# Optimization experiments

Measured on AMD Instinct MI355X. Metric: run time of the kernel, lower is better.

Reference implementation:

```python
import jax, jax.numpy as jnp
import numpy as np

EPS = 1e-20


def _conv(x, w, pad):
    # NCHW / OIHW conv, stride 1, symmetric padding
    return jax.lax.conv_general_dilated(
        x, w, window_strides=(1, 1),
        padding=((pad, pad), (pad, pad)),
        dimension_numbers=("NCHW", "OIHW", "NCHW"))


def _nconv(data, conf, w, b, pad):
    # normalized convolution: conv(d*c)/conv(c) + bias ; cout = conv(c)/sum(w)
    denom = _conv(conf, w, pad)
    nomin = _conv(data * conf, w, pad)
    out = nomin / (denom + EPS) + b[None, :, None, None]
    s = jnp.sum(w, axis=(1, 2, 3))  # per-out-channel kernel sum
    cout = denom / s[None, :, None, None]
    return out, cout


def _maxpool_ds(x, c):
    # 2x2/stride-2 max pool on c, gathering x at argmax positions (torch return_indices semantics)
    B, C, H, W = c.shape
    cw = c.reshape(B, C, H // 2, 2, W // 2, 2).transpose(0, 1, 2, 4, 3, 5).reshape(B, C, H // 2, W // 2, 4)
    xw = x.reshape(B, C, H // 2, 2, W // 2, 2).transpose(0, 1, 2, 4, 3, 5).reshape(B, C, H // 2, W // 2, 4)
    idx = jnp.argmax(cw, axis=-1)  # first-max tie-break, same as torch
    c_ds = jnp.take_along_axis(cw, idx[..., None], axis=-1)[..., 0] / 4.0
    x_ds = jnp.take_along_axis(xw, idx[..., None], axis=-1)[..., 0]
    return x_ds, c_ds


def _up2(x):
    return jnp.repeat(jnp.repeat(x, 2, axis=2), 2, axis=3)


def setup_inputs() -> dict:
    key = jax.random.key(0)
    ks = jax.random.split(key, 18)
    B, H, W = 8, 512, 512
    x0 = jax.random.normal(ks[0], (B, 1, H, W), dtype=jnp.float32)
    c0 = jax.random.uniform(ks[1], (B, 1, H, W), dtype=jnp.float32)

    def posw(k, shape):
        # positive kernel (the module enforces positivity via softplus hook)
        return jax.nn.softplus(jax.random.normal(k, shape, dtype=jnp.float32))

    inp = {"x0": x0, "c0": c0}
    shapes = {
        "w1": (2, 1, 5, 5), "w2": (2, 2, 5, 5), "w3": (2, 2, 5, 5),
        "w4": (2, 4, 3, 3), "w5": (2, 4, 3, 3), "w6": (2, 4, 3, 3),
        "w7": (1, 2, 1, 1),
    }
    for i, (name, shp) in enumerate(shapes.items()):
        inp[name] = posw(ks[2 + i], shp)
        inp["b" + name[1:]] = jnp.full((shp[0],), 0.01, dtype=jnp.float32)
    return inp


def reference(x0, c0, w1, b1, w2, b2, w3, b3, w4, b4, w5, b5, w6, b6, w7, b7):
    x1, c1 = _nconv(x0, c0, w1, b1, 2)
    x1, c1 = _nconv(x1, c1, w2, b2, 2)
    x1, c1 = _nconv(x1, c1, w3, b3, 2)

    x1_ds, c1_ds = _maxpool_ds(x1, c1)
    x2_ds, c2_ds = _nconv(x1_ds, c1_ds, w2, b2, 2)
    x2_ds, c2_ds = _nconv(x2_ds, c2_ds, w3, b3, 2)

    x2_dss, c2_dss = _maxpool_ds(x2_ds, c2_ds)
    x3_ds, c3_ds = _nconv(x2_dss, c2_dss, w2, b2, 2)

    x3_dss, c3_dss = _maxpool_ds(x3_ds, c3_ds)
    x4_ds, c4_ds = _nconv(x3_dss, c3_dss, w2, b2, 2)

    x4, c4 = _up2(x4_ds), _up2(c4_ds)
    x34_ds, c34_ds = _nconv(jnp.concatenate((x3_ds, x4), 1), jnp.concatenate((c3_ds, c4), 1), w4, b4, 1)

    x34, c34 = _up2(x34_ds), _up2(c34_ds)
    x23_ds, c23_ds = _nconv(jnp.concatenate((x2_ds, x34), 1), jnp.concatenate((c2_ds, c34), 1), w5, b5, 1)

    x23, c23 = _up2(x23_ds), _up2(c23_ds)
    xout, cout = _nconv(jnp.concatenate((x23, x1), 1), jnp.concatenate((c23, c1), 1), w6, b6, 1)
    xout, cout = _nconv(xout, cout, w7, b7, 0)
    return xout, cout
```

## Files before the change

kernel.cpp:

```cpp
#include <hip/hip_runtime.h>

#define EPSF 1e-20f

typedef float v2f __attribute__((ext_vector_type(2)));

__device__ __forceinline__ float frcp(float x) { return __builtin_amdgcn_rcpf(x); }


struct CD8 { v2f v[8]; };
__device__ __forceinline__ CD8 load_cd8(const float2* p) {
    const float4* q = (const float4*)p;
    const float4 t0 = q[0], t1 = q[1], t2 = q[2], t3 = q[3];
    CD8 r;
    r.v[0] = (v2f){t0.x, t0.y}; r.v[1] = (v2f){t0.z, t0.w};
    r.v[2] = (v2f){t1.x, t1.y}; r.v[3] = (v2f){t1.z, t1.w};
    r.v[4] = (v2f){t2.x, t2.y}; r.v[5] = (v2f){t2.z, t2.w};
    r.v[6] = (v2f){t3.x, t3.y}; r.v[7] = (v2f){t3.z, t3.w};
    return r;
}
struct CD6 { v2f v[6]; };
__device__ __forceinline__ CD6 load_cd6(const float2* p) {
    const float4* q = (const float4*)p;
    const float4 t0 = q[0], t1 = q[1], t2 = q[2];
    CD6 r;
    r.v[0] = (v2f){t0.x, t0.y}; r.v[1] = (v2f){t0.z, t0.w};
    r.v[2] = (v2f){t1.x, t1.y}; r.v[3] = (v2f){t1.z, t1.w};
    r.v[4] = (v2f){t2.x, t2.y}; r.v[5] = (v2f){t2.z, t2.w};
    return r;
}
__device__ __forceinline__ void fma2(v2f& a, float w, v2f cd) {
    a = __builtin_elementwise_fma((v2f){w, w}, cd, a);
}

template<int NCI, int CI0, int CINT, int K, int ROWS>
__device__ __forceinline__ void conv_core_i(const float2* __restrict__ s,
                                            const float* __restrict__ wgt,
                                            int lh, int lw,
                                            v2f acc[2][4])
{
    constexpr int JB = 2 - (K / 2);
    #pragma unroll
    for (int kh = 0; kh < K; ++kh) {
        #pragma unroll
        for (int ci = 0; ci < NCI; ++ci) {
            const CD8 cd = load_cd8(s + (ci * ROWS + lh + kh) * 72 + lw + 2);
            #pragma unroll
            for (int kw = 0; kw < K; ++kw) {
                const float w0 = wgt[((0 * CINT + CI0 + ci) * K + kh) * K + kw];
                const float w1 = wgt[((1 * CINT + CI0 + ci) * K + kh) * K + kw];
                #pragma unroll
                for (int p = 0; p < 4; ++p) {
                    const int j = p + kw + JB;
                    fma2(acc[0][p], w0, cd.v[j]);
                    fma2(acc[1][p], w1, cd.v[j]);
                }
            }
        }
    }
}

template<int LO0>
__device__ __forceinline__ void conv_low_i(const float2* __restrict__ s_lo,
                                           const float* __restrict__ wgt,
                                           int lh, int lw,
                                           v2f acc[2][4])
{
    #pragma unroll
    for (int kh = 0; kh < 3; ++kh) {
        const int rel_r = ((lh + kh - 1) >> 1) + 1;
        #pragma unroll
        for (int lci = 0; lci < 2; ++lci) {
            const CD6 cd = load_cd6(s_lo + (lci * 10 + rel_r) * 40 + (lw >> 1) + 2);
            #pragma unroll
            for (int kw = 0; kw < 3; ++kw) {
                const float w0 = wgt[((0 * 4 + LO0 + lci) * 3 + kh) * 3 + kw];
                const float w1 = wgt[((1 * 4 + LO0 + lci) * 3 + kh) * 3 + kw];
                #pragma unroll
                for (int p = 0; p < 4; ++p) {
                    const int t = p + kw - 1;
                    const int jl = ((t < 0) ? -1 : (t >> 1)) + 2;
                    fma2(acc[0][p], w0, cd.v[jl]);
                    fma2(acc[1][p], w1, cd.v[jl]);
                }
            }
        }
    }
}

template<int CINT, int K>
__device__ __forceinline__ void nconv_epilogue_i(const float* __restrict__ wgt,
                                                 const float* __restrict__ bias,
                                                 v2f acc[2][4],
                                                 float4 uo[2], float4 co4[2])
{
    #pragma unroll
    for (int c = 0; c < 2; ++c) {
        float s = 0.f;
        for (int i = 0; i < CINT * K * K; ++i) s += wgt[c * CINT * K * K + i];
        const float is = 1.0f / s;
        const float bb = bias[c];
        #pragma unroll
        for (int p = 0; p < 4; ++p) {
            const float xo = acc[c][p].y * frcp(acc[c][p].x + EPSF) + bb;
            const float cv = acc[c][p].x * is;
            (&co4[c].x)[p] = cv;
            (&uo[c].x)[p]  = xo * cv;
        }
    }
}

__global__ __launch_bounds__(256)
void enc12_fused(const float* __restrict__ x0, const float* __restrict__ c0,
                 const float* __restrict__ wA, const float* __restrict__ bA,
                 const float* __restrict__ wB, const float* __restrict__ bB,
                 float* __restrict__ uout, float* __restrict__ cout)
{
    __shared__ __align__(16) float2 in_cd[24][84];
    __shared__ __align__(16) float2 mid_cd[2][20][72];

    const int tid = threadIdx.x;
    const int bw = blockIdx.x * 64;
    const int bh = blockIdx.y * 16;
    const int b  = blockIdx.z;

    const float4* x4 = (const float4*)x0;
    const float4* c4 = (const float4*)c0;
    for (int i = tid; i < 480; i += 256) {
        const int r = i / 20, k = i % 20;
        const int gh = bh - 4 + r;
        const int gw4 = (bw >> 2) - 2 + k;
        float4 xx = make_float4(0.f, 0.f, 0.f, 0.f);
        float4 cc = make_float4(0.f, 0.f, 0.f, 0.f);
        if ((unsigned)gh < 512u && (unsigned)gw4 < 128u) {
            const int a = (b << 16) + (gh << 7) + gw4;
            xx = x4[a];
            cc = c4[a];
        }
        float4* dst = (float4*)&in_cd[r][4 * k];
        dst[0] = make_float4(cc.x, xx.x * cc.x, cc.y, xx.y * cc.y);
        dst[1] = make_float4(cc.z, xx.z * cc.z, cc.w, xx.w * cc.w);
    }

    float isA0, isA1;
    {
        float s0 = 0.f, s1 = 0.f;
        for (int i = 0; i < 25; ++i) { s0 += wA[i]; s1 += wA[25 + i]; }
        isA0 = 1.0f / s0;
        isA1 = 1.0f / s1;
    }
    __syncthreads();

    #pragma unroll
    for (int pass = 0; pass < 2; ++pass) {
        int r, g;
        bool active = true;
        if (pass == 0) { r = tid >> 4; g = tid & 15; }
        else {
            if (tid < 64) { r = 16 + (tid >> 4); g = tid & 15; }
            else if (tid < 104) { const int t = tid - 64; r = t >> 1; g = 16 + (t & 1); }
            else { active = false; r = 0; g = 0; }
        }
        if (active) {
            v2f acc[2][4];
            #pragma unroll
            for (int c = 0; c < 2; ++c)
                #pragma unroll
                for (int p = 0; p < 4; ++p) acc[c][p] = (v2f){0.f, 0.f};
            #pragma unroll
            for (int kh = 0; kh < 5; ++kh) {
                const CD8 cd = load_cd8(&in_cd[r + kh][4 * g + 2]);
                #pragma unroll
                for (int kw = 0; kw < 5; ++kw) {
                    const float w0 = wA[kh * 5 + kw];
                    const float w1 = wA[25 + kh * 5 + kw];
                    #pragma unroll
                    for (int p = 0; p < 4; ++p) {
                        fma2(acc[0][p], w0, cd.v[p + kw]);
                        fma2(acc[1][p], w1, cd.v[p + kw]);
                    }
                }
            }
            const int orow = bh + r - 2;
            const bool rok = (unsigned)orow < 512u;
            #pragma unroll
            for (int c = 0; c < 2; ++c) {
                const float is = (c == 0) ? isA0 : isA1;
                float cv[4], du[4];
                #pragma unroll
                for (int p = 0; p < 4; ++p) {
                    const int ocol = bw + 4 * g - 4 + p;
                    const bool ok = rok && (unsigned)ocol < 512u;
                    const float xo = acc[c][p].y * frcp(acc[c][p].x + EPSF) + bA[c];
                    const float v = acc[c][p].x * is;
                    cv[p] = ok ? v : 0.f;
                    du[p] = ok ? xo * v : 0.f;
                }
                float4* dst = (float4*)&mid_cd[c][r][4 * g];
                dst[0] = make_float4(cv[0], du[0], cv[1], du[1]);
                dst[1] = make_float4(cv[2], du[2], cv[3], du[3]);
            }
        }
    }
    __syncthreads();

    const int lh = tid >> 4;
    const int lw = (tid & 15) << 2;
    v2f acc[2][4];
    #pragma unroll
    for (int c = 0; c < 2; ++c)
        #pragma unroll
        for (int p = 0; p < 4; ++p) acc[c][p] = (v2f){0.f, 0.f};

    conv_core_i<2, 0, 2, 5, 20>(&mid_cd[0][0][0], wB, lh, lw, acc);

    float4 uo[2], co4[2];
    nconv_epilogue_i<2, 5>(wB, bB, acc, uo, co4);

    const int oh = bh + lh;
    #pragma unroll
    for (int c = 0; c < 2; ++c) {
        const int a = ((b * 2 + c) << 16) + (oh << 7) + ((bw + lw) >> 2);
        ((float4*)uout)[a] = uo[c];
        ((float4*)cout)[a] = co4[c];
    }
}

__global__ __launch_bounds__(256)
void enc45_fused(const float* __restrict__ inU, const float* __restrict__ inC,
                 const float* __restrict__ wA, const float* __restrict__ bA,
                 const float* __restrict__ wB, const float* __restrict__ bB,
                 float* __restrict__ uout, float* __restrict__ cout,
                 float* __restrict__ poolU, float* __restrict__ poolC)
{
    __shared__ __align__(16) float2 in_cd[2][24][84];
    __shared__ __align__(16) float2 mid_cd[2][20][72];

    const int tid = threadIdx.x;
    const int bw = blockIdx.x * 64;
    const int bh = blockIdx.y * 16;
    const int b  = blockIdx.z;

    const float4* U4 = (const float4*)inU;
    const float4* C4 = (const float4*)inC;
    for (int i = tid; i < 960; i += 256) {
        const int ci = i / 480;
        const int r = (i / 20) % 24, k = i % 20;
        const int gh = bh - 4 + r;
        const int gw4 = (bw >> 2) - 2 + k;
        float4 dd = make_float4(0.f, 0.f, 0.f, 0.f);
        float4 cc = make_float4(0.f, 0.f, 0.f, 0.f);
        if ((unsigned)gh < 256u && (unsigned)gw4 < 64u) {
            const int a = ((b * 2 + ci) << 14) + (gh << 6) + gw4;
            dd = U4[a];
            cc = C4[a];
        }
        float4* dst = (float4*)&in_cd[ci][r][4 * k];
        dst[0] = make_float4(cc.x, dd.x, cc.y, dd.y);
        dst[1] = make_float4(cc.z, dd.z, cc.w, dd.w);
    }

    float isA0, isA1;
    {
        float s0 = 0.f, s1 = 0.f;
        for (int i = 0; i < 50; ++i) { s0 += wA[i]; s1 += wA[50 + i]; }
        isA0 = 1.0f / s0;
        isA1 = 1.0f / s1;
    }
    __syncthreads();

    #pragma unroll
    for (int pass = 0; pass < 2; ++pass) {
        int r, g;
        bool active = true;
        if (pass == 0) { r = tid >> 4; g = tid & 15; }
        else {
            if (tid < 64) { r = 16 + (tid >> 4); g = tid & 15; }
            else if (tid < 104) { const int t = tid - 64; r = t >> 1; g = 16 + (t & 1); }
            else { active = false; r = 0; g = 0; }
        }
        if (active) {
            v2f acc[2][4];
            #pragma unroll
            for (int c = 0; c < 2; ++c)
                #pragma unroll
                for (int p = 0; p < 4; ++p) acc[c][p] = (v2f){0.f, 0.f};
            #pragma unroll
            for (int kh = 0; kh < 5; ++kh) {
                #pragma unroll
                for (int ci = 0; ci < 2; ++ci) {
                    const CD8 cd = load_cd8(&in_cd[ci][r + kh][4 * g + 2]);
                    #pragma unroll
                    for (int kw = 0; kw < 5; ++kw) {
                        const float w0 = wA[((0 * 2 + ci) * 5 + kh) * 5 + kw];
                        const float w1 = wA[((1 * 2 + ci) * 5 + kh) * 5 + kw];
                        #pragma unroll
                        for (int p = 0; p < 4; ++p) {
                            fma2(acc[0][p], w0, cd.v[p + kw]);
                            fma2(acc[1][p], w1, cd.v[p + kw]);
                        }
                    }
                }
            }
            const int orow = bh + r - 2;
            const bool rok = (unsigned)orow < 256u;
            #pragma unroll
            for (int c = 0; c < 2; ++c) {
                const float is = (c == 0) ? isA0 : isA1;
                float cv[4], du[4];
                #pragma unroll
                for (int p = 0; p < 4; ++p) {
                    const int ocol = bw + 4 * g - 4 + p;
                    const bool ok = rok && (unsigned)ocol < 256u;
                    const float xo = acc[c][p].y * frcp(acc[c][p].x + EPSF) + bA[c];
                    const float v = acc[c][p].x * is;
                    cv[p] = ok ? v : 0.f;
                    du[p] = ok ? xo * v : 0.f;
                }
                float4* dst = (float4*)&mid_cd[c][r][4 * g];
                dst[0] = make_float4(cv[0], du[0], cv[1], du[1]);
                dst[1] = make_float4(cv[2], du[2], cv[3], du[3]);
            }
        }
    }
    __syncthreads();

    const int lh = tid >> 4;
    const int lw = (tid & 15) << 2;
    v2f acc[2][4];
    #pragma unroll
    for (int c = 0; c < 2; ++c)
        #pragma unroll
        for (int p = 0; p < 4; ++p) acc[c][p] = (v2f){0.f, 0.f};

    conv_core_i<2, 0, 2, 5, 20>(&mid_cd[0][0][0], wB, lh, lw, acc);

    float4 uo[2], co4[2];
    nconv_epilogue_i<2, 5>(wB, bB, acc, uo, co4);

    const int oh = bh + lh;
    #pragma unroll
    for (int c = 0; c < 2; ++c) {
        const int a = ((b * 2 + c) << 14) + (oh << 6) + ((bw + lw) >> 2);
        ((float4*)uout)[a] = uo[c];
        ((float4*)cout)[a] = co4[c];
    }

    __syncthreads();
    float2* pb = &mid_cd[0][0][0];
    #pragma unroll
    for (int c = 0; c < 2; ++c) {
        float2* row = pb + (c * 16 + lh) * 64 + lw;
        #pragma unroll
        for (int p = 0; p < 4; ++p)
            row[p] = make_float2((&co4[c].x)[p], (&uo[c].x)[p]);
    }
    __syncthreads();
    #pragma unroll
    for (int rep = 0; rep < 2; ++rep) {
        const int o = tid + rep * 256;
        const int ch = o >> 8;
        const int idx = o & 255;
        const int pr = idx >> 5;
        const int pcc = idx & 31;
        const float2* base = pb + (ch * 16 + 2 * pr) * 64 + 2 * pcc;
        const float2 a0 = base[0], a1 = base[1], a2 = base[64], a3 = base[65];
        float m = a0.x, g = a0.y;
        if (a1.x > m) { m = a1.x; g = a1.y; }
        if (a2.x > m) { m = a2.x; g = a2.y; }
        if (a3.x > m) { m = a3.x; g = a3.y; }
        const int pa = ((b * 2 + ch) << 14) + (((bh >> 1) + pr) << 7) + (bw >> 1) + pcc;
        poolU[pa] = g * 0.25f;
        poolC[pa] = m * 0.25f;
    }
}

__global__ __launch_bounds__(256)
void mid_kern(const float* __restrict__ p2U, const float* __restrict__ p2C,
              const float* __restrict__ w2, const float* __restrict__ b2,
              const float* __restrict__ w4, const float* __restrict__ b4,
              float* __restrict__ x34U, float* __restrict__ x34C)
{
    __shared__ __align__(16) float2 sp_cd[2][32][88];
    __shared__ __align__(16) float2 sx3_cd[2][28][80];
    __shared__ __align__(16) float2 sp3_cd[2][14][48];
    __shared__ __align__(16) float2 sx4_cd[2][10][40];

    const int tid = threadIdx.x;
    const int bw = blockIdx.x * 64;
    const int bh = blockIdx.y * 16;
    const int b = blockIdx.z;

    const float4* U4 = (const float4*)p2U;
    const float4* C4 = (const float4*)p2C;
    for (int i = tid; i < 2 * 32 * 22; i += 256) {
        const int ci = i / 704;
        const int r  = (i / 22) % 32;
        const int cf = i % 22;
        const int gh = bh - 8 + r;
        const int gw4 = (bw >> 2) - 3 + cf;
        float4 dd = make_float4(0.f, 0.f, 0.f, 0.f);
        float4 cc = make_float4(0.f, 0.f, 0.f, 0.f);
        if ((unsigned)gh < 128u && (unsigned)gw4 < 32u) {
            const int a = ((b * 2 + ci) << 12) + (gh << 5) + gw4;
            dd = U4[a];
            cc = C4[a];
        }
        float4* dst = (float4*)&sp_cd[ci][r][cf * 4];
        dst[0] = make_float4(cc.x, dd.x, cc.y, dd.y);
        dst[1] = make_float4(cc.z, dd.z, cc.w, dd.w);
    }
    __syncthreads();

    {
        float s2[2];
        #pragma unroll
        for (int c = 0; c < 2; ++c) {
            float s = 0.f;
            for (int i = 0; i < 50; ++i) s += w2[c * 50 + i];
            s2[c] = 1.0f / s;
        }
        for (int s = tid; s < 560; s += 256) {
            const int r = s / 20;
            const int g = s % 20;
            v2f acc[2][4];
            #pragma unroll
            for (int c = 0; c < 2; ++c)
                #pragma unroll
                for (int p = 0; p < 4; ++p) acc[c][p] = (v2f){0.f, 0.f};
            #pragma unroll
            for (int kh = 0; kh < 5; ++kh) {
                #pragma unroll
                for (int ci = 0; ci < 2; ++ci) {
                    const CD8 cd = load_cd8(&sp_cd[ci][r + kh][4 * g + 2]);
                    #pragma unroll
                    for (int kw = 0; kw < 5; ++kw) {
                        const float w0 = w2[((0 * 2 + ci) * 5 + kh) * 5 + kw];
                        const float w1 = w2[((1 * 2 + ci) * 5 + kh) * 5 + kw];
                        #pragma unroll
                        for (int p = 0; p < 4; ++p) {
                            fma2(acc[0][p], w0, cd.v[p + kw]);
                            fma2(acc[1][p], w1, cd.v[p + kw]);
                        }
                    }
                }
            }
            const int orow = bh - 6 + r;
            const bool rok = (unsigned)orow < 128u;
            #pragma unroll
            for (int c = 0; c < 2; ++c) {
                float cv[4], du[4];
                #pragma unroll
                for (int p = 0; p < 4; ++p) {
                    const int ocol = bw - 8 + 4 * g + p;
                    const bool ok = rok && (unsigned)ocol < 128u;
                    const float xo = acc[c][p].y * frcp(acc[c][p].x + EPSF) + b2[c];
                    const float v = acc[c][p].x * s2[c];
                    cv[p] = ok ? v : 0.f;
                    du[p] = ok ? xo * v : 0.f;
                }
                float4* dst = (float4*)&sx3_cd[c][r][4 * g];
                dst[0] = make_float4(cv[0], du[0], cv[1], du[1]);
                dst[1] = make_float4(cv[2], du[2], cv[3], du[3]);
            }
        }
    }
    __syncthreads();

    for (int i = tid; i < 2 * 14 * 48; i += 256) {
        const int ch = i / 672;
        const int r  = (i / 48) % 14;
        const int c  = i % 48;
        const int R = (bh >> 1) - 3 + r;
        const int C = (bw >> 1) - 8 + c;
        float g = 0.f, m = 0.f;
        if (c >= 4 && c < 44 && (unsigned)R < 64u && (unsigned)C < 64u) {
            const int xr = 2 * r, xc = 2 * c - 8;
            const float2 a0 = sx3_cd[ch][xr][xc],     a1 = sx3_cd[ch][xr][xc + 1];
            const float2 a2 = sx3_cd[ch][xr + 1][xc], a3 = sx3_cd[ch][xr + 1][xc + 1];
            m = a0.x; g = a0.y;
            if (a1.x > m) { m = a1.x; g = a1.y; }
            if (a2.x > m) { m = a2.x; g = a2.y; }
            if (a3.x > m) { m = a3.x; g = a3.y; }
            g *= 0.25f; m *= 0.25f;
        }
        sp3_cd[ch][r][c] = make_float2(m, g);
    }
    __syncthreads();

    {
        float s2[2];
        #pragma unroll
        for (int c = 0; c < 2; ++c) {
            float s = 0.f;
            for (int i = 0; i < 50; ++i) s += w2[c * 50 + i];
            s2[c] = 1.0f / s;
        }
        for (int s = tid; s < 100; s += 256) {
            const int r = s / 10;
            const int g = s % 10;
            v2f acc[2][4];
            #pragma unroll
            for (int c = 0; c < 2; ++c)
                #pragma unroll
                for (int p = 0; p < 4; ++p) acc[c][p] = (v2f){0.f, 0.f};
            #pragma unroll
            for (int kh = 0; kh < 5; ++kh) {
                #pragma unroll
                for (int ci = 0; ci < 2; ++ci) {
                    const CD8 cd = load_cd8(&sp3_cd[ci][r + kh][4 * g + 2]);
                    #pragma unroll
                    for (int kw = 0; kw < 5; ++kw) {
                        const float w0 = w2[((0 * 2 + ci) * 5 + kh) * 5 + kw];
                        const float w1 = w2[((1 * 2 + ci) * 5 + kh) * 5 + kw];
                        #pragma unroll
                        for (int p = 0; p < 4; ++p) {
                            fma2(acc[0][p], w0, cd.v[p + kw]);
                            fma2(acc[1][p], w1, cd.v[p + kw]);
                        }
                    }
                }
            }
            const int orow = (bh >> 1) - 1 + r;
            const bool rok = (unsigned)orow < 64u;
            #pragma unroll
            for (int c = 0; c < 2; ++c) {
                float cv[4], du[4];
                #pragma unroll
                for (int p = 0; p < 4; ++p) {
                    const int ocol = (bw >> 1) - 4 + 4 * g + p;
                    const bool ok = rok && (unsigned)ocol < 64u;
                    const float xo = acc[c][p].y * frcp(acc[c][p].x + EPSF) + b2[c];
                    const float v = acc[c][p].x * s2[c];
                    cv[p] = ok ? v : 0.f;
                    du[p] = ok ? xo * v : 0.f;
                }
                float4* dst = (float4*)&sx4_cd[c][r][4 * g];
                dst[0] = make_float4(cv[0], du[0], cv[1], du[1]);
                dst[1] = make_float4(cv[2], du[2], cv[3], du[3]);
            }
        }
    }
    __syncthreads();

    {
        const int lh = tid >> 4;
        const int lw = (tid & 15) << 2;
        v2f acc[2][4];
        #pragma unroll
        for (int c = 0; c < 2; ++c)
            #pragma unroll
            for (int p = 0; p < 4; ++p) acc[c][p] = (v2f){0.f, 0.f};

        #pragma unroll
        for (int kh = 0; kh < 3; ++kh) {
            #pragma unroll
            for (int ci = 0; ci < 2; ++ci) {
                const CD8 cd = load_cd8(&sx3_cd[ci][lh + kh + 5][lw + 6]);
                #pragma unroll
                for (int kw = 0; kw < 3; ++kw) {
                    const float w0 = w4[((0 * 4 + ci) * 3 + kh) * 3 + kw];
                    const float w1 = w4[((1 * 4 + ci) * 3 + kh) * 3 + kw];
                    #pragma unroll
                    for (int p = 0; p < 4; ++p) {
                        const int j = p + kw + 1;
                        fma2(acc[0][p], w0, cd.v[j]);
                        fma2(acc[1][p], w1, cd.v[j]);
                    }
                }
            }
        }
        conv_low_i<2>(&sx4_cd[0][0][0], w4, lh, lw, acc);

        float4 uo[2], co4[2];
        nconv_epilogue_i<4, 3>(w4, b4, acc, uo, co4);
        #pragma unroll
        for (int c = 0; c < 2; ++c) {
            const int a = ((b * 2 + c) << 12) + ((bh + lh) << 5) + ((bw + lw) >> 2);
            ((float4*)x34U)[a] = uo[c];
            ((float4*)x34C)[a] = co4[c];
        }
    }
}

template<int CIN, int K, int LOGHW, bool IN_IS_U, bool POOL>
__global__ __launch_bounds__(256)
void nconv_tiled(const float* __restrict__ xin, const float* __restrict__ cin_,
                 const float* __restrict__ wgt, const float* __restrict__ bias,
                 float* __restrict__ uout, float* __restrict__ cout,
                 float* __restrict__ poolU, float* __restrict__ poolC)
{
    constexpr int HW = 1 << LOGHW;
    constexpr int PAD = K / 2;
    constexpr int TH = 16;
    constexpr int ROWS = TH + 2 * PAD;
    constexpr int NC4 = 18;
    __shared__ __align__(16) float2 s_cd[CIN][ROWS][72];

    const int tid = threadIdx.x;
    const int base_w = blockIdx.x * 64;
    const int base_h = blockIdx.y * TH;
    const int b = blockIdx.z;

    constexpr int SLOTS = CIN * ROWS * NC4;
    const float4* x4 = (const float4*)xin;
    const float4* c4p = (const float4*)cin_;
    for (int i = tid; i < SLOTS; i += 256) {
        const int ci = i / (ROWS * NC4);
        const int r  = (i / NC4) % ROWS;
        const int cf = i % NC4;
        const int gh = base_h - PAD + r;
        const int gw4 = (base_w >> 2) + cf - 1;
        float4 dd = make_float4(0.f, 0.f, 0.f, 0.f);
        float4 cc = make_float4(0.f, 0.f, 0.f, 0.f);
        if ((unsigned)gh < (unsigned)HW && (unsigned)gw4 < (unsigned)(HW >> 2)) {
            const int a = ((b * CIN + ci) << (2 * LOGHW - 2)) + (gh << (LOGHW - 2)) + gw4;
            const float4 xx = x4[a];
            cc = c4p[a];
            if (IN_IS_U) dd = xx;
            else dd = make_float4(xx.x * cc.x, xx.y * cc.y, xx.z * cc.z, xx.w * cc.w);
        }
        float4* dst = (float4*)&s_cd[ci][r][cf * 4];
        dst[0] = make_float4(cc.x, dd.x, cc.y, dd.y);
        dst[1] = make_float4(cc.z, dd.z, cc.w, dd.w);
    }
    __syncthreads();

    const int lh = tid >> 4;
    const int lw = (tid & 15) << 2;
    v2f acc[2][4];
    #pragma unroll
    for (int c = 0; c < 2; ++c)
        #pragma unroll
        for (int p = 0; p < 4; ++p) acc[c][p] = (v2f){0.f, 0.f};

    conv_core_i<CIN, 0, CIN, K, ROWS>(&s_cd[0][0][0], wgt, lh, lw, acc);

    float4 uo[2], co4[2];
    nconv_epilogue_i<CIN, K>(wgt, bias, acc, uo, co4);

    const int oh = base_h + lh;
    #pragma unroll
    for (int c = 0; c < 2; ++c) {
        const int a = ((b * 2 + c) << (2 * LOGHW - 2)) + (oh << (LOGHW - 2)) + ((base_w + lw) >> 2);
        ((float4*)uout)[a] = uo[c];
        ((float4*)cout)[a] = co4[c];
    }

    if (POOL) {
        __syncthreads();
        float2* pb = &s_cd[0][0][0];
        #pragma unroll
        for (int c = 0; c < 2; ++c) {
            float2* row = pb + (c * 16 + lh) * 64 + lw;
            #pragma unroll
            for (int p = 0; p < 4; ++p)
                row[p] = make_float2((&co4[c].x)[p], (&uo[c].x)[p]);
        }
        __syncthreads();
        #pragma unroll
        for (int rep = 0; rep < 2; ++rep) {
            const int o = tid + rep * 256;
            const int ch = o >> 8;
            const int idx = o & 255;
            const int pr = idx >> 5;
            const int pcc = idx & 31;
            const float2* base = pb + (ch * 16 + 2 * pr) * 64 + 2 * pcc;
            const float2 a0 = base[0], a1 = base[1], a2 = base[64], a3 = base[65];
            float m = a0.x, g = a0.y;
            if (a1.x > m) { m = a1.x; g = a1.y; }
            if (a2.x > m) { m = a2.x; g = a2.y; }
            if (a3.x > m) { m = a3.x; g = a3.y; }
            const int pa = ((b * 2 + ch) << (2 * (LOGHW - 1)))
                         + (((base_h >> 1) + pr) << (LOGHW - 1)) + (base_w >> 1) + pcc;
            poolU[pa] = g * 0.25f;
            poolC[pa] = m * 0.25f;
        }
    }
}

template<bool UP_FIRST, int LOGHW, bool FINAL>
__global__ __launch_bounds__(256)
void nconv_cat_tiled(const float* __restrict__ skU, const float* __restrict__ skC,
                     const float* __restrict__ loU, const float* __restrict__ loC,
                     const float* __restrict__ wgt, const float* __restrict__ bias,
                     float* __restrict__ uout, float* __restrict__ cout,
                     const float* __restrict__ w7, const float* __restrict__ b7)
{
    constexpr int HW = 1 << LOGHW;
    constexpr int HWL = HW >> 1;
    constexpr int TH = 16;
    constexpr int ROWS = TH + 2;
    constexpr int NC4 = 18;
    constexpr int SK0 = UP_FIRST ? 2 : 0;
    constexpr int LO0 = UP_FIRST ? 0 : 2;
    __shared__ __align__(16) float2 s_cd[2][ROWS][72];
    __shared__ __align__(16) float2 lo_cd[2][10][40];

    const int tid = threadIdx.x;
    const int base_w = blockIdx.x * 64;
    const int base_h = blockIdx.y * TH;
    const int b = blockIdx.z;

    constexpr int SLOTS = 2 * ROWS * NC4;
    const float4* sU4 = (const float4*)skU;
    const float4* sC4 = (const float4*)skC;
    for (int i = tid; i < SLOTS; i += 256) {
        const int ci = i / (ROWS * NC4);
        const int r  = (i / NC4) % ROWS;
        const int cf = i % NC4;
        const int gh = base_h - 1 + r;
        const int gw4 = (base_w >> 2) + cf - 1;
        float4 dd = make_float4(0.f, 0.f, 0.f, 0.f);
        float4 cc = make_float4(0.f, 0.f, 0.f, 0.f);
        if ((unsigned)gh < (unsigned)HW && (unsigned)gw4 < (unsigned)(HW >> 2)) {
            const int a = ((b * 2 + ci) << (2 * LOGHW - 2)) + (gh << (LOGHW - 2)) + gw4;
            dd = sU4[a];
            cc = sC4[a];
        }
        float4* dst = (float4*)&s_cd[ci][r][cf * 4];
        dst[0] = make_float4(cc.x, dd.x, cc.y, dd.y);
        dst[1] = make_float4(cc.z, dd.z, cc.w, dd.w);
    }
    constexpr int LO_SLOTS = 2 * 10 * 10;
    const int lo_r0 = (base_h >> 1) - 1;
    const int lo_c4_0 = (base_w >> 3) - 1;
    const float4* lU4 = (const float4*)loU;
    const float4* lC4 = (const float4*)loC;
    for (int i = tid; i < LO_SLOTS; i += 256) {
        const int ci = i / 100;
        const int r  = (i / 10) % 10;
        const int cf = i % 10;
        const int gr = lo_r0 + r;
        const int gc4 = lo_c4_0 + cf;
        float4 dd = make_float4(0.f, 0.f, 0.f, 0.f);
        float4 cc = make_float4(0.f, 0.f, 0.f, 0.f);
        if ((unsigned)gr < (unsigned)HWL && (unsigned)gc4 < (unsigned)(HWL >> 2)) {
            const int a = ((b * 2 + ci) << (2 * (LOGHW - 1) - 2)) + (gr << (LOGHW - 3)) + gc4;
            dd = lU4[a];
            cc = lC4[a];
        }
        float4* dst = (float4*)&lo_cd[ci][r][cf * 4];
        dst[0] = make_float4(cc.x, dd.x, cc.y, dd.y);
        dst[1] = make_float4(cc.z, dd.z, cc.w, dd.w);
    }
    __syncthreads();

    const int lh = tid >> 4;
    const int lw = (tid & 15) << 2;
    v2f acc[2][4];
    #pragma unroll
    for (int c = 0; c < 2; ++c)
        #pragma unroll
        for (int p = 0; p < 4; ++p) acc[c][p] = (v2f){0.f, 0.f};

    conv_core_i<2, SK0, 4, 3, ROWS>(&s_cd[0][0][0], wgt, lh, lw, acc);
    conv_low_i<LO0>(&lo_cd[0][0][0], wgt, lh, lw, acc);

    float4 uo[2], co4[2];
    nconv_epilogue_i<4, 3>(wgt, bias, acc, uo, co4);

    const int oh = base_h + lh;
    if (FINAL) {
        const float w70 = w7[0], w71 = w7[1], bb7 = b7[0];
        const float inv = frcp(w70 + w71);
        float4 xo4, cc4;
        #pragma unroll
        for (int p = 0; p < 4; ++p) {
            const float d1 = w70 * (&co4[0].x)[p] + w71 * (&co4[1].x)[p];
            (&xo4.x)[p] = (w70 * (&uo[0].x)[p] + w71 * (&uo[1].x)[p]) * frcp(d1 + EPSF) + bb7;
            (&cc4.x)[p] = d1 * inv;
        }
        const int a = (b << (2 * LOGHW - 2)) + (oh << (LOGHW - 2)) + ((base_w + lw) >> 2);
        ((float4*)uout)[a] = xo4;
        ((float4*)uout)[(1 << 19) + a] = cc4;
    } else {
        #pragma unroll
        for (int c = 0; c < 2; ++c) {
            const int a = ((b * 2 + c) << (2 * LOGHW - 2)) + (oh << (LOGHW - 2)) + ((base_w + lw) >> 2);
            ((float4*)uout)[a] = uo[c];
            ((float4*)cout)[a] = co4[c];
        }
    }
}

extern "C" void kernel_launch(void* const* d_in, const int* in_sizes, int n_in,
                              void* d_out, int out_size, void* d_ws, size_t ws_size,
                              hipStream_t stream) {
    (void)in_sizes; (void)n_in; (void)out_size; (void)ws_size;
    const float* x0 = (const float*)d_in[0];
    const float* c0 = (const float*)d_in[1];
    const float* w1 = (const float*)d_in[2];  const float* b1 = (const float*)d_in[3];
    const float* w2 = (const float*)d_in[4];  const float* b2 = (const float*)d_in[5];
    const float* w3 = (const float*)d_in[6];  const float* b3 = (const float*)d_in[7];
    const float* w4 = (const float*)d_in[8];  const float* b4 = (const float*)d_in[9];
    const float* w5 = (const float*)d_in[10]; const float* b5 = (const float*)d_in[11];
    const float* w6 = (const float*)d_in[12]; const float* b6 = (const float*)d_in[13];
    const float* w7 = (const float*)d_in[14]; const float* b7 = (const float*)d_in[15];

    float* ws = (float*)d_ws;
    const size_t S512 = 8ull * 2 * 512 * 512;
    const size_t S256 = 8ull * 2 * 256 * 256;
    const size_t S128 = 8ull * 2 * 128 * 128;

    float* X1x = ws;            float* X1c = ws + S512;
    float* Ax  = ws + 2 * S512;
    float* Bx  = ws + 4 * S512; float* Bc  = ws + 5 * S512;
    float* x23x = Ax;               float* x23c = Ax + S256;
    float* x2x  = Ax + 2 * S256;    float* x2c  = Ax + 3 * S256;
    float* p1x  = Ax + 4 * S256;    float* p1c  = Ax + 5 * S256;
    float* p2x  = Bx + 2 * S128;    float* p2c  = Bx + 3 * S128;
    float* x34x = Bx + 4 * S128;    float* x34c = Bx + 5 * S128;

    enc12_fused<<<dim3(8, 32, 8), 256, 0, stream>>>(
        x0, c0, w1, b1, w2, b2, Bx, Bc);
    nconv_tiled<2, 5, 9, true, true><<<dim3(8, 32, 8), 256, 0, stream>>>(
        Bx, Bc, w3, b3, X1x, X1c, p1x, p1c);
    enc45_fused<<<dim3(4, 16, 8), 256, 0, stream>>>(
        p1x, p1c, w2, b2, w3, b3, x2x, x2c, p2x, p2c);
    mid_kern<<<dim3(2, 8, 8), 256, 0, stream>>>(
        p2x, p2c, w2, b2, w4, b4, x34x, x34c);
    nconv_cat_tiled<false, 8, false><<<dim3(4, 16, 8), 256, 0, stream>>>(
        x2x, x2c, x34x, x34c, w5, b5, x23x, x23c, nullptr, nullptr);
    nconv_cat_tiled<true, 9, true><<<dim3(8, 32, 8), 256, 0, stream>>>(
        X1x, X1c, x23x, x23c, w6, b6, (float*)d_out, nullptr, w7, b7);
}
```

Baseline: 114.0 us.

## Register-block two output rows per thread and pool from registers in the first encoder stages

The first two full-resolution kernels now use 32-row tiles. Each thread computes two adjacent output rows, so every input row loaded from shared memory feeds both row accumulators, and the 5x5 halo is amortised over a taller tile. The third-conv kernel replaces the generic templated kernel and does the 2x2 max-pool directly from the thread's own register results. This removes the shared-memory staging pass and its two extra barriers. In exchange, accumulator registers double and enc12 needs about 67KB of shared memory, which may lower occupancy.

```diff
diff --git a/kernel.cpp b/kernel.cpp
--- a/kernel.cpp
+++ b/kernel.cpp
@@ -110,22 +110,23 @@
 }
 
 __global__ __launch_bounds__(256)
-void enc12_fused(const float* __restrict__ x0, const float* __restrict__ c0,
-                 const float* __restrict__ wA, const float* __restrict__ bA,
-                 const float* __restrict__ wB, const float* __restrict__ bB,
-                 float* __restrict__ uout, float* __restrict__ cout)
+void enc12_blk(const float* __restrict__ x0, const float* __restrict__ c0,
+               const float* __restrict__ w1_, const float* __restrict__ b1_,
+               const float* __restrict__ w2_, const float* __restrict__ b2_,
+               float* __restrict__ uout, float* __restrict__ cout)
 {
-    __shared__ __align__(16) float2 in_cd[24][84];
-    __shared__ __align__(16) float2 mid_cd[2][20][72];
+    __shared__ __align__(16) float2 smem[8384];
+    float2* inb = smem;
+    float2* m1  = smem + 3200;
 
     const int tid = threadIdx.x;
     const int bw = blockIdx.x * 64;
-    const int bh = blockIdx.y * 16;
+    const int bh = blockIdx.y * 32;
     const int b  = blockIdx.z;
 
     const float4* x4 = (const float4*)x0;
     const float4* c4 = (const float4*)c0;
-    for (int i = tid; i < 480; i += 256) {
+    for (int i = tid; i < 800; i += 256) {
         const int r = i / 20, k = i % 20;
         const int gh = bh - 4 + r;
         const int gw4 = (bw >> 2) - 2 + k;
@@ -136,92 +137,238 @@
             xx = x4[a];
             cc = c4[a];
         }
-        float4* dst = (float4*)&in_cd[r][4 * k];
+        float4* dst = (float4*)(inb + r * 80 + 4 * k);
         dst[0] = make_float4(cc.x, xx.x * cc.x, cc.y, xx.y * cc.y);
         dst[1] = make_float4(cc.z, xx.z * cc.z, cc.w, xx.w * cc.w);
     }
 
-    float isA0, isA1;
+    float is1[2], is2[2];
     {
         float s0 = 0.f, s1 = 0.f;
-        for (int i = 0; i < 25; ++i) { s0 += wA[i]; s1 += wA[25 + i]; }
-        isA0 = 1.0f / s0;
-        isA1 = 1.0f / s1;
+        for (int i = 0; i < 25; ++i) { s0 += w1_[i]; s1 += w1_[25 + i]; }
+        is1[0] = 1.0f / s0; is1[1] = 1.0f / s1;
+        float t0 = 0.f, t1 = 0.f;
+        for (int i = 0; i < 50; ++i) { t0 += w2_[i]; t1 += w2_[50 + i]; }
+        is2[0] = 1.0f / t0; is2[1] = 1.0f / t1;
     }
     __syncthreads();
 
     #pragma unroll
     for (int pass = 0; pass < 2; ++pass) {
-        int r, g;
-        bool active = true;
-        if (pass == 0) { r = tid >> 4; g = tid & 15; }
-        else {
-            if (tid < 64) { r = 16 + (tid >> 4); g = tid & 15; }
-            else if (tid < 104) { const int t = tid - 64; r = t >> 1; g = 16 + (t & 1); }
-            else { active = false; r = 0; g = 0; }
-        }
-        if (active) {
-            v2f acc[2][4];
+        const int item = tid + pass * 256;
+        if (item < 324) {
+            const int rp = item / 18;
+            const int g  = item % 18;
+            v2f acc[2][2][4];
             #pragma unroll
             for (int c = 0; c < 2; ++c)
                 #pragma unroll
-                for (int p = 0; p < 4; ++p) acc[c][p] = (v2f){0.f, 0.f};
-            #pragma unroll
-            for (int kh = 0; kh < 5; ++kh) {
-                const CD8 cd = load_cd8(&in_cd[r + kh][4 * g + 2]);
-                #pragma unroll
-                for (int kw = 0; kw < 5; ++kw) {
-                    const float w0 = wA[kh * 5 + kw];
-                    const float w1 = wA[25 + kh * 5 + kw];
+                for (int o = 0; o < 2; ++o)
+                    #pragma unroll
+                    for (int p = 0; p < 4; ++p) acc[c][o][p] = (v2f){0.f, 0.f};
+            #pragma unroll
+            for (int j = 0; j < 6; ++j) {
+                const CD8 cd = load_cd8(inb + (2 * rp + j) * 80 + 4 * g + 2);
+                #pragma unroll
+                for (int o = 0; o < 2; ++o) {
+                    const int kh = j - o;
+                    if (kh < 0 || kh > 4) continue;
+                    #pragma unroll
+                    for (int kw = 0; kw < 5; ++kw) {
+                        const float wa = w1_[kh * 5 + kw];
+                        const float wb = w1_[25 + kh * 5 + kw];
+                        #pragma unroll
+                        for (int p = 0; p < 4; ++p) {
+                            fma2(acc[0][o][p], wa, cd.v[p + kw]);
+                            fma2(acc[1][o][p], wb, cd.v[p + kw]);
+                        }
+                    }
+                }
+            }
+            #pragma unroll
+            for (int o = 0; o < 2; ++o) {
+                const int grow = bh - 2 + 2 * rp + o;
+                const bool rok = (unsigned)grow < 512u;
+                #pragma unroll
+                for (int c = 0; c < 2; ++c) {
+                    float cv[4], du[4];
                     #pragma unroll
                     for (int p = 0; p < 4; ++p) {
-                        fma2(acc[0][p], w0, cd.v[p + kw]);
-                        fma2(acc[1][p], w1, cd.v[p + kw]);
+                        const int ocol = bw - 4 + 4 * g + p;
+                        const bool ok = rok && (unsigned)ocol < 512u;
+                        const float xo = acc[c][o][p].y * frcp(acc[c][o][p].x + EPSF) + b1_[c];
+                        const float v = acc[c][o][p].x * is1[c];
+                        cv[p] = ok ? v : 0.f;
+                        du[p] = ok ? xo * v : 0.f;
                     }
-                }
-            }
-            const int orow = bh + r - 2;
-            const bool rok = (unsigned)orow < 512u;
-            #pragma unroll
-            for (int c = 0; c < 2; ++c) {
-                const float is = (c == 0) ? isA0 : isA1;
-                float cv[4], du[4];
-                #pragma unroll
-                for (int p = 0; p < 4; ++p) {
-                    const int ocol = bw + 4 * g - 4 + p;
-                    const bool ok = rok && (unsigned)ocol < 512u;
-                    const float xo = acc[c][p].y * frcp(acc[c][p].x + EPSF) + bA[c];
-                    const float v = acc[c][p].x * is;
-                    cv[p] = ok ? v : 0.f;
-                    du[p] = ok ? xo * v : 0.f;
-                }
-                float4* dst = (float4*)&mid_cd[c][r][4 * g];
-                dst[0] = make_float4(cv[0], du[0], cv[1], du[1]);
-                dst[1] = make_float4(cv[2], du[2], cv[3], du[3]);
-            }
-        }
-    }
-    __syncthreads();
-
-    const int lh = tid >> 4;
-    const int lw = (tid & 15) << 2;
-    v2f acc[2][4];
+                    float4* dst = (float4*)(m1 + (c * 36 + 2 * rp + o) * 72 + 4 * g);
+                    dst[0] = make_float4(cv[0], du[0], cv[1], du[1]);
+                    dst[1] = make_float4(cv[2], du[2], cv[3], du[3]);
+                }
+            }
+        }
+    }
+    __syncthreads();
+
+    const int tx = tid & 15;
+    const int ty = tid >> 4;
+    v2f acc[2][2][4];
     #pragma unroll
     for (int c = 0; c < 2; ++c)
         #pragma unroll
-        for (int p = 0; p < 4; ++p) acc[c][p] = (v2f){0.f, 0.f};
-
-    conv_core_i<2, 0, 2, 5, 20>(&mid_cd[0][0][0], wB, lh, lw, acc);
-
-    float4 uo[2], co4[2];
-    nconv_epilogue_i<2, 5>(wB, bB, acc, uo, co4);
-
-    const int oh = bh + lh;
+        for (int o = 0; o < 2; ++o)
+            #pragma unroll
+            for (int p = 0; p < 4; ++p) acc[c][o][p] = (v2f){0.f, 0.f};
+
+    #pragma unroll
+    for (int j = 0; j < 6; ++j) {
+        #pragma unroll
+        for (int ci = 0; ci < 2; ++ci) {
+            const CD8 cd = load_cd8(m1 + (ci * 36 + 2 * ty + j) * 72 + 4 * tx + 2);
+            #pragma unroll
+            for (int o = 0; o < 2; ++o) {
+                const int kh = j - o;
+                if (kh < 0 || kh > 4) continue;
+                #pragma unroll
+                for (int kw = 0; kw < 5; ++kw) {
+                    const float wa = w2_[((0 * 2 + ci) * 5 + kh) * 5 + kw];
+                    const float wb = w2_[((1 * 2 + ci) * 5 + kh) * 5 + kw];
+                    #pragma unroll
+                    for (int p = 0; p < 4; ++p) {
+                        fma2(acc[0][o][p], wa, cd.v[p + kw]);
+                        fma2(acc[1][o][p], wb, cd.v[p + kw]);
+                    }
+                }
+            }
+        }
+    }
+    #pragma unroll
+    for (int o = 0; o < 2; ++o)
+        #pragma unroll
+        for (int c = 0; c < 2; ++c) {
+            float4 uo, co;
+            #pragma unroll
+            for (int p = 0; p < 4; ++p) {
+                const float xo = acc[c][o][p].y * frcp(acc[c][o][p].x + EPSF) + b2_[c];
+                const float cv = acc[c][o][p].x * is2[c];
+                (&co.x)[p] = cv;
+                (&uo.x)[p] = xo * cv;
+            }
+            const int a = ((b * 2 + c) << 16) + ((bh + 2 * ty + o) << 7) + (bw >> 2) + tx;
+            ((float4*)uout)[a] = uo;
+            ((float4*)cout)[a] = co;
+        }
+}
+
+__global__ __launch_bounds__(256)
+void enc3_blk(const float* __restrict__ inU, const float* __restrict__ inC,
+              const float* __restrict__ wgt, const float* __restrict__ bias,
+              float* __restrict__ X1u, float* __restrict__ X1c,
+              float* __restrict__ p1u, float* __restrict__ p1c)
+{
+    __shared__ __align__(16) float2 s_cd[2][36][72];
+
+    const int tid = threadIdx.x;
+    const int bw = blockIdx.x * 64;
+    const int bh = blockIdx.y * 32;
+    const int b  = blockIdx.z;
+
+    const float4* U4 = (const float4*)inU;
+    const float4* C4 = (const float4*)inC;
+    for (int i = tid; i < 1296; i += 256) {
+        const int ci = i / 648;
+        const int r  = (i / 18) % 36;
+        const int k  = i % 18;
+        const int gh = bh - 2 + r;
+        const int gw4 = (bw >> 2) - 1 + k;
+        float4 dd = make_float4(0.f, 0.f, 0.f, 0.f);
+        float4 cc = make_float4(0.f, 0.f, 0.f, 0.f);
+        if ((unsigned)gh < 512u && (unsigned)gw4 < 128u) {
+            const int a = ((b * 2 + ci) << 16) + (gh << 7) + gw4;
+            dd = U4[a];
+            cc = C4[a];
+        }
+        float4* dst = (float4*)&s_cd[ci][r][4 * k];
+        dst[0] = make_float4(cc.x, dd.x, cc.y, dd.y);
+        dst[1] = make_float4(cc.z, dd.z, cc.w, dd.w);
+    }
+
+    float is3[2];
+    {
+        float s0 = 0.f, s1 = 0.f;
+        for (int i = 0; i < 50; ++i) { s0 += wgt[i]; s1 += wgt[50 + i]; }
+        is3[0] = 1.0f / s0; is3[1] = 1.0f / s1;
+    }
+    __syncthreads();
+
+    const int tx = tid & 15;
+    const int ty = tid >> 4;
+    v2f acc[2][2][4];
+    #pragma unroll
+    for (int c = 0; c < 2; ++c)
+        #pragma unroll
+        for (int o = 0; o < 2; ++o)
+            #pragma unroll
+            for (int p = 0; p < 4; ++p) acc[c][o][p] = (v2f){0.f, 0.f};
+
+    #pragma unroll
+    for (int j = 0; j < 6; ++j) {
+        #pragma unroll
+        for (int ci = 0; ci < 2; ++ci) {
+            const CD8 cd = load_cd8(&s_cd[ci][2 * ty + j][4 * tx + 2]);
+            #pragma unroll
+            for (int o = 0; o < 2; ++o) {
+                const int kh = j - o;
+                if (kh < 0 || kh > 4) continue;
+                #pragma unroll
+                for (int kw = 0; kw < 5; ++kw) {
+                    const float wa = wgt[((0 * 2 + ci) * 5 + kh) * 5 + kw];
+                    const float wb = wgt[((1 * 2 + ci) * 5 + kh) * 5 + kw];
+                    #pragma unroll
+                    for (int p = 0; p < 4; ++p) {
+                        fma2(acc[0][o][p], wa, cd.v[p + kw]);
+                        fma2(acc[1][o][p], wb, cd.v[p + kw]);
+                    }
+                }
+            }
+        }
+    }
+
+    float cv[2][2][4], du[2][2][4];
+    #pragma unroll
+    for (int c = 0; c < 2; ++c)
+        #pragma unroll
+        for (int o = 0; o < 2; ++o) {
+            float4 uo, co;
+            #pragma unroll
+            for (int p = 0; p < 4; ++p) {
+                const float xo = acc[c][o][p].y * frcp(acc[c][o][p].x + EPSF) + bias[c];
+                const float v = acc[c][o][p].x * is3[c];
+                cv[c][o][p] = v;
+                du[c][o][p] = xo * v;
+                (&co.x)[p] = v;
+                (&uo.x)[p] = xo * v;
+            }
+            const int a = ((b * 2 + c) << 16) + ((bh + 2 * ty + o) << 7) + (bw >> 2) + tx;
+            ((float4*)X1u)[a] = uo;
+            ((float4*)X1c)[a] = co;
+        }
+
     #pragma unroll
     for (int c = 0; c < 2; ++c) {
-        const int a = ((b * 2 + c) << 16) + (oh << 7) + ((bw + lw) >> 2);
-        ((float4*)uout)[a] = uo[c];
-        ((float4*)cout)[a] = co4[c];
+        float pg[2], pm[2];
+        #pragma unroll
+        for (int pc = 0; pc < 2; ++pc) {
+            float m = cv[c][0][2 * pc], g = du[c][0][2 * pc];
+            if (cv[c][0][2 * pc + 1] > m) { m = cv[c][0][2 * pc + 1]; g = du[c][0][2 * pc + 1]; }
+            if (cv[c][1][2 * pc]     > m) { m = cv[c][1][2 * pc];     g = du[c][1][2 * pc]; }
+            if (cv[c][1][2 * pc + 1] > m) { m = cv[c][1][2 * pc + 1]; g = du[c][1][2 * pc + 1]; }
+            pg[pc] = g * 0.25f;
+            pm[pc] = m * 0.25f;
+        }
+        const int pa = ((b * 2 + c) << 16) + (((bh >> 1) + ty) << 8) + (bw >> 1) + 2 * tx;
+        *(float2*)&p1u[pa] = make_float2(pg[0], pg[1]);
+        *(float2*)&p1c[pa] = make_float2(pm[0], pm[1]);
     }
 }
 
@@ -578,102 +725,6 @@
             const int a = ((b * 2 + c) << 12) + ((bh + lh) << 5) + ((bw + lw) >> 2);
             ((float4*)x34U)[a] = uo[c];
             ((float4*)x34C)[a] = co4[c];
-        }
-    }
-}
-
-template<int CIN, int K, int LOGHW, bool IN_IS_U, bool POOL>
-__global__ __launch_bounds__(256)
-void nconv_tiled(const float* __restrict__ xin, const float* __restrict__ cin_,
-                 const float* __restrict__ wgt, const float* __restrict__ bias,
-                 float* __restrict__ uout, float* __restrict__ cout,
-                 float* __restrict__ poolU, float* __restrict__ poolC)
-{
-    constexpr int HW = 1 << LOGHW;
-    constexpr int PAD = K / 2;
-    constexpr int TH = 16;
-    constexpr int ROWS = TH + 2 * PAD;
-    constexpr int NC4 = 18;
-    __shared__ __align__(16) float2 s_cd[CIN][ROWS][72];
-
-    const int tid = threadIdx.x;
-    const int base_w = blockIdx.x * 64;
-    const int base_h = blockIdx.y * TH;
-    const int b = blockIdx.z;
-
-    constexpr int SLOTS = CIN * ROWS * NC4;
-    const float4* x4 = (const float4*)xin;
-    const float4* c4p = (const float4*)cin_;
-    for (int i = tid; i < SLOTS; i += 256) {
-        const int ci = i / (ROWS * NC4);
-        const int r  = (i / NC4) % ROWS;
-        const int cf = i % NC4;
-        const int gh = base_h - PAD + r;
-        const int gw4 = (base_w >> 2) + cf - 1;
-        float4 dd = make_float4(0.f, 0.f, 0.f, 0.f);
-        float4 cc = make_float4(0.f, 0.f, 0.f, 0.f);
-        if ((unsigned)gh < (unsigned)HW && (unsigned)gw4 < (unsigned)(HW >> 2)) {
-            const int a = ((b * CIN + ci) << (2 * LOGHW - 2)) + (gh << (LOGHW - 2)) + gw4;
-            const float4 xx = x4[a];
-            cc = c4p[a];
-            if (IN_IS_U) dd = xx;
-            else dd = make_float4(xx.x * cc.x, xx.y * cc.y, xx.z * cc.z, xx.w * cc.w);
-        }
-        float4* dst = (float4*)&s_cd[ci][r][cf * 4];
-        dst[0] = make_float4(cc.x, dd.x, cc.y, dd.y);
-        dst[1] = make_float4(cc.z, dd.z, cc.w, dd.w);
-    }
-    __syncthreads();
-
-    const int lh = tid >> 4;
-    const int lw = (tid & 15) << 2;
-    v2f acc[2][4];
-    #pragma unroll
-    for (int c = 0; c < 2; ++c)
-        #pragma unroll
-        for (int p = 0; p < 4; ++p) acc[c][p] = (v2f){0.f, 0.f};
-
-    conv_core_i<CIN, 0, CIN, K, ROWS>(&s_cd[0][0][0], wgt, lh, lw, acc);
-
-    float4 uo[2], co4[2];
-    nconv_epilogue_i<CIN, K>(wgt, bias, acc, uo, co4);
-
-    const int oh = base_h + lh;
-    #pragma unroll
-    for (int c = 0; c < 2; ++c) {
-        const int a = ((b * 2 + c) << (2 * LOGHW - 2)) + (oh << (LOGHW - 2)) + ((base_w + lw) >> 2);
-        ((float4*)uout)[a] = uo[c];
-        ((float4*)cout)[a] = co4[c];
-    }
-
-    if (POOL) {
-        __syncthreads();
-        float2* pb = &s_cd[0][0][0];
-        #pragma unroll
-        for (int c = 0; c < 2; ++c) {
-            float2* row = pb + (c * 16 + lh) * 64 + lw;
-            #pragma unroll
-            for (int p = 0; p < 4; ++p)
-                row[p] = make_float2((&co4[c].x)[p], (&uo[c].x)[p]);
-        }
-        __syncthreads();
-        #pragma unroll
-        for (int rep = 0; rep < 2; ++rep) {
-            const int o = tid + rep * 256;
-            const int ch = o >> 8;
-            const int idx = o & 255;
-            const int pr = idx >> 5;
-            const int pcc = idx & 31;
-            const float2* base = pb + (ch * 16 + 2 * pr) * 64 + 2 * pcc;
-            const float2 a0 = base[0], a1 = base[1], a2 = base[64], a3 = base[65];
-            float m = a0.x, g = a0.y;
-            if (a1.x > m) { m = a1.x; g = a1.y; }
-            if (a2.x > m) { m = a2.x; g = a2.y; }
-            if (a3.x > m) { m = a3.x; g = a3.y; }
-            const int pa = ((b * 2 + ch) << (2 * (LOGHW - 1)))
-                         + (((base_h >> 1) + pr) << (LOGHW - 1)) + (base_w >> 1) + pcc;
-            poolU[pa] = g * 0.25f;
-            poolC[pa] = m * 0.25f;
         }
     }
 }
@@ -811,9 +862,9 @@
     float* p2x  = Bx + 2 * S128;    float* p2c  = Bx + 3 * S128;
     float* x34x = Bx + 4 * S128;    float* x34c = Bx + 5 * S128;
 
-    enc12_fused<<<dim3(8, 32, 8), 256, 0, stream>>>(
+    enc12_blk<<<dim3(8, 16, 8), 256, 0, stream>>>(
         x0, c0, w1, b1, w2, b2, Bx, Bc);
-    nconv_tiled<2, 5, 9, true, true><<<dim3(8, 32, 8), 256, 0, stream>>>(
+    enc3_blk<<<dim3(8, 16, 8), 256, 0, stream>>>(
         Bx, Bc, w3, b3, X1x, X1c, p1x, p1c);
     enc45_fused<<<dim3(4, 16, 8), 256, 0, stream>>>(
         p1x, p1c, w2, b2, w3, b3, x2x, x2c, p2x, p2c);
```

New measurement: 120.4 us. +5.6%, slower.
